# Kernel tuning notes

Measured on AMD Instinct MI355X. Metric: run time of the kernel, lower is better.

## Reference

```python
import math
import jax, jax.numpy as jnp
import numpy as np

B, T, C, H = 4, 2048, 1024, 16
D = C // H  # head dim = 64


def setup_inputs() -> dict:
    key = jax.random.key(0)
    ks = jax.random.split(key, 5)
    s = 0.02  # trunc_normal-like init scale
    return {
        "x":  jax.random.normal(ks[0], (B, T, C), dtype=jnp.float32),
        "wq": jax.random.normal(ks[1], (C, C), dtype=jnp.float32) * s,
        "bq": jnp.zeros((C,), dtype=jnp.float32),
        "wk": jax.random.normal(ks[2], (C, C), dtype=jnp.float32) * s,
        "bk": jnp.zeros((C,), dtype=jnp.float32),
        "wv": jax.random.normal(ks[3], (C, C), dtype=jnp.float32) * s,
        "bv": jnp.zeros((C,), dtype=jnp.float32),
        "wp": jax.random.normal(ks[4], (C, C), dtype=jnp.float32) * s,
        "bp": jnp.zeros((C,), dtype=jnp.float32),
    }


def reference(x, wq, bq, wk, bk, wv, bv, wp, bp):
    b, t, c = x.shape
    # QKV projections -> (B, H, T, D)
    q = (x @ wq + bq).reshape(b, t, H, D).transpose(0, 2, 1, 3)
    k = (x @ wk + bk).reshape(b, t, H, D).transpose(0, 2, 1, 3)
    v = (x @ wv + bv).reshape(b, t, H, D).transpose(0, 2, 1, 3)
    present = jnp.stack((k, v))  # (2, B, H, T, D)
    # scaled dot-product with causal mask (layer_past is None path)
    att = jnp.einsum('bhqd,bhkd->bhqk', q, k) * (1.0 / math.sqrt(D))
    causal = jnp.tril(jnp.ones((t, t), dtype=bool))  # (T, T)
    att = jnp.where(causal[None, None], att, -jnp.inf)
    att = jax.nn.softmax(att, axis=-1)
    # dropout prob = 0.0 (eval) -> identity
    y = jnp.einsum('bhqk,bhkd->bhqd', att, v)
    y = y.transpose(0, 2, 1, 3).reshape(b, t, c)
    y = y @ wp + bp
    return (y, present)
```

## Files before the change

kernel.cpp:

```cpp
#include <hip/hip_runtime.h>
#include <hip/hip_bf16.h>
#include <stdint.h>

typedef unsigned short u16;
typedef __bf16 bf16x8 __attribute__((ext_vector_type(8)));
typedef float f32x4 __attribute__((ext_vector_type(4)));

#define BB 4
#define TT 2048
#define CC 1024
#define HH 16
#define DD 64

__device__ __forceinline__ u16 f2bf(float f) {
  union { float f; unsigned int u; } v; v.f = f;
  unsigned int u = v.u;
  unsigned int r = (u + 0x7fffu + ((u >> 16) & 1u)) >> 16;
  return (u16)r;
}

__device__ __forceinline__ void async_copy16(const void* g, void* l) {
  __builtin_amdgcn_global_load_lds(
      (const __attribute__((address_space(1))) void*)g,
      (__attribute__((address_space(3))) void*)l, 16, 0, 0);
}

__global__ __launch_bounds__(256) void k_cast_x(const float* __restrict__ x,
                                                u16* __restrict__ xb) {
  int i = (blockIdx.x * 256 + threadIdx.x) * 4;
  float4 f = *reinterpret_cast<const float4*>(x + i);
  ushort4 o;
  o.x = f2bf(f.x); o.y = f2bf(f.y); o.z = f2bf(f.z); o.w = f2bf(f.w);
  *reinterpret_cast<ushort4*>(xb + i) = o;
}

__global__ __launch_bounds__(256) void k_transpose_w(
    const float* __restrict__ w0, const float* __restrict__ w1,
    const float* __restrict__ w2, const float* __restrict__ w3,
    u16* __restrict__ t0, u16* __restrict__ t1,
    u16* __restrict__ t2, u16* __restrict__ t3) {
  const float* w = blockIdx.z == 0 ? w0 : blockIdx.z == 1 ? w1 : blockIdx.z == 2 ? w2 : w3;
  u16* t = blockIdx.z == 0 ? t0 : blockIdx.z == 1 ? t1 : blockIdx.z == 2 ? t2 : t3;
  __shared__ u16 tile[32][33];
  int tx = threadIdx.x, ty = threadIdx.y;
  int k0 = blockIdx.x * 32, n0 = blockIdx.y * 32;
#pragma unroll
  for (int r = 0; r < 4; r++)
    tile[ty + r * 8][tx] = f2bf(w[(size_t)(k0 + ty + r * 8) * CC + n0 + tx]);
  __syncthreads();
#pragma unroll
  for (int r = 0; r < 4; r++)
    t[(size_t)(n0 + ty + r * 8) * CC + k0 + tx] = tile[tx][ty + r * 8];
}

__global__ __launch_bounds__(256) void k_transpose_v(
    const float* __restrict__ out_v, u16* __restrict__ vbt) {
  int tb = blockIdx.x * 64;
  int bh = blockIdx.y;
  const float* src = out_v + (size_t)bh * TT * DD;
  u16* dst = vbt + (size_t)bh * TT * DD;
  __shared__ u16 tile[64][65];
  int tid = threadIdx.x;
#pragma unroll
  for (int p = 0; p < 4; p++) {
    int c = p * 256 + tid;
    int t = c >> 4, d0 = (c & 15) * 4;
    float4 f = *reinterpret_cast<const float4*>(src + (size_t)(tb + t) * DD + d0);
    tile[t][d0 + 0] = f2bf(f.x);
    tile[t][d0 + 1] = f2bf(f.y);
    tile[t][d0 + 2] = f2bf(f.z);
    tile[t][d0 + 3] = f2bf(f.w);
  }
  __syncthreads();
#pragma unroll
  for (int p = 0; p < 2; p++) {
    int c = p * 256 + tid;
    int d = c >> 3, t0 = (c & 7) * 8;
    ushort4 lo, hi;
    lo.x = tile[t0 + 0][d]; lo.y = tile[t0 + 1][d];
    lo.z = tile[t0 + 2][d]; lo.w = tile[t0 + 3][d];
    hi.x = tile[t0 + 4][d]; hi.y = tile[t0 + 5][d];
    hi.z = tile[t0 + 6][d]; hi.w = tile[t0 + 7][d];
    u16* o = dst + (size_t)d * TT + tb + t0;
    *reinterpret_cast<ushort4*>(o) = lo;
    *reinterpret_cast<ushort4*>(o + 4) = hi;
  }
}

#define GEMM_PROLOGUE()                                                        \
  int tid = threadIdx.x;                                                       \
  int lane = tid & 63;                                                         \
  int wave = tid >> 6;                                                         \
  int l15 = lane & 15, quad = lane >> 4;                                       \
  int wave_m = wave & 1, wave_n = wave >> 1;                                   \
  __shared__ u16 lA[128 * 32];                                                 \
  __shared__ u16 lB[128 * 32];                                                 \
  f32x4 acc[4][4] = {};                                                        \
  for (int k0 = 0; k0 < CC; k0 += 32) {                                        \
    __syncthreads();                                                           \
    _Pragma("unroll")                                                          \
    for (int r = 0; r < 2; r++) {                                              \
      int c = r * 256 + tid;                                                   \
      int row = c >> 2, col8 = (c & 3) * 8;                                    \
      async_copy16(A + (size_t)(tile_m + row) * CC + k0 + col8, &lA[c * 8]);   \
    }                                                                          \
    _Pragma("unroll")                                                          \
    for (int r = 0; r < 2; r++) {                                              \
      int c = r * 256 + tid;                                                   \
      int row = c >> 2, col8 = (c & 3) * 8;                                    \
      async_copy16(Bt + (size_t)(tile_n + row) * CC + k0 + col8, &lB[c * 8]);  \
    }                                                                          \
    __syncthreads();                                                           \
    bf16x8 af[4], bfr[4];                                                      \
    _Pragma("unroll")                                                          \
    for (int i = 0; i < 4; i++)                                                \
      af[i] = *reinterpret_cast<const bf16x8*>(                                \
          &lA[(wave_m * 64 + i * 16 + l15) * 32 + quad * 8]);                  \
    _Pragma("unroll")                                                          \
    for (int j = 0; j < 4; j++)                                                \
      bfr[j] = *reinterpret_cast<const bf16x8*>(                               \
          &lB[(wave_n * 64 + j * 16 + l15) * 32 + quad * 8]);                  \
    _Pragma("unroll")                                                          \
    for (int i = 0; i < 4; i++)                                                \
      _Pragma("unroll")                                                        \
      for (int j = 0; j < 4; j++)                                              \
        acc[i][j] =                                                            \
            __builtin_amdgcn_mfma_f32_16x16x32_bf16(af[i], bfr[j], acc[i][j],  \
                                                    0, 0, 0);                  \
  }

__global__ __launch_bounds__(256) void k_gemm_qkv(
    const u16* __restrict__ xb,
    const u16* __restrict__ wtq, const u16* __restrict__ wtk, const u16* __restrict__ wtv,
    const float* __restrict__ bq, const float* __restrict__ bk, const float* __restrict__ bv,
    u16* __restrict__ qb, u16* __restrict__ kb,
    float* __restrict__ out_k, float* __restrict__ out_v) {
  int mat = blockIdx.z;
  const u16* A = xb;
  const u16* Bt = mat == 0 ? wtq : mat == 1 ? wtk : wtv;
  const float* bias = mat == 0 ? bq : mat == 1 ? bk : bv;
  int tile_m = blockIdx.x * 128;
  int tile_n = blockIdx.y * 128;

  GEMM_PROLOGUE()

#pragma unroll
  for (int j = 0; j < 4; j++) {
    int n = tile_n + wave_n * 64 + j * 16 + l15;
    int h = n >> 6, d = n & 63;
    float bias_n = bias[n];
#pragma unroll
    for (int i = 0; i < 4; i++) {
#pragma unroll
      for (int r = 0; r < 4; r++) {
        int m = tile_m + wave_m * 64 + i * 16 + quad * 4 + r;
        int b = m >> 11, t = m & 2047;
        float val = acc[i][j][r] + bias_n;
        size_t idx = (((size_t)(b * HH + h)) * TT + t) * DD + d;
        if (mat == 0) {
          qb[idx] = f2bf(val);
        } else if (mat == 1) {
          out_k[idx] = val;
          kb[idx] = f2bf(val);
        } else {
          out_v[idx] = val;
        }
      }
    }
  }
}

__global__ __launch_bounds__(256) void k_gemm_proj(
    const u16* __restrict__ yb, const u16* __restrict__ wtp,
    const float* __restrict__ bp, float* __restrict__ out) {
  const u16* A = yb;
  const u16* Bt = wtp;
  int tile_m = blockIdx.x * 128;
  int tile_n = blockIdx.y * 128;

  GEMM_PROLOGUE()

#pragma unroll
  for (int j = 0; j < 4; j++) {
    int n = tile_n + wave_n * 64 + j * 16 + l15;
    float bias_n = bp[n];
#pragma unroll
    for (int i = 0; i < 4; i++) {
#pragma unroll
      for (int r = 0; r < 4; r++) {
        int m = tile_m + wave_m * 64 + i * 16 + quad * 4 + r;
        out[(size_t)m * CC + n] = acc[i][j][r] + bias_n;
      }
    }
  }
}

__global__ __launch_bounds__(256) void k_attn(
    const u16* __restrict__ qb, const u16* __restrict__ kbuf,
    const u16* __restrict__ vtb, u16* __restrict__ yatt) {
  int qpair = blockIdx.x;
  int bh = blockIdx.y;
  int tid = threadIdx.x;
  int lane = tid & 63;
  int wave = tid >> 6;
  int l15 = lane & 15, quad = lane >> 4;

  const u16* Q = qb + (size_t)bh * TT * DD;
  const u16* K = kbuf + (size_t)bh * TT * DD;
  const u16* Vt = vtb + (size_t)bh * TT * DD;

  __shared__ u16 kl[2][64 * 64];
  __shared__ u16 vl[2][64 * 64];
  __shared__ u16 pl[4][16 * 64];
  u16* plw = pl[wave];

  int h = bh & 15, b = bh >> 4;

  int c0 = tid, c1 = tid + 256;
  int r0 = c0 >> 3, e0 = (((c0 & 7) * 16) ^ ((r0 & 7) << 4)) >> 1;
  int r1 = c1 >> 3, e1 = (((c1 & 7) * 16) ^ ((r1 & 7) << 4)) >> 1;

  auto stage = [&](int buf, int kb0) {
    async_copy16(K + (size_t)(kb0 + r0) * DD + e0, &kl[buf][c0 * 8]);
    async_copy16(K + (size_t)(kb0 + r1) * DD + e1, &kl[buf][c1 * 8]);
    async_copy16(Vt + (size_t)r0 * TT + kb0 + e0, &vl[buf][c0 * 8]);
    async_copy16(Vt + (size_t)r1 * TT + kb0 + e1, &vl[buf][c1 * 8]);
  };

#pragma unroll
  for (int side = 0; side < 2; side++) {
    int qt = side == 0 ? qpair : 31 - qpair;

    int qr = qt * 64 + wave * 16 + l15;
    bf16x8 qf0 = *reinterpret_cast<const bf16x8*>(Q + (size_t)qr * DD + quad * 8);
    bf16x8 qf1 = *reinterpret_cast<const bf16x8*>(Q + (size_t)qr * DD + 32 + quad * 8);

    f32x4 o_acc[4] = {};
    float m_run[4], l_run[4];
#pragma unroll
    for (int r = 0; r < 4; r++) { m_run[r] = -1e30f; l_run[r] = 0.f; }

    stage(0, 0);

    for (int kblk = 0; kblk <= qt; kblk++) {
      int cur = kblk & 1;
      if (kblk < qt) {
        stage(cur ^ 1, (kblk + 1) * 64);
        asm volatile("s_waitcnt vmcnt(4)" ::: "memory");
      } else {
        asm volatile("s_waitcnt vmcnt(0)" ::: "memory");
      }
      __builtin_amdgcn_sched_barrier(0);
      __builtin_amdgcn_s_barrier();
      __builtin_amdgcn_sched_barrier(0);

      f32x4 s_acc[4];
#pragma unroll
      for (int nb = 0; nb < 4; nb++) {
        int krow = nb * 16 + l15;
        int xr = (krow & 7) << 4;
        const u16* kp = &kl[cur][krow * 64];
        bf16x8 kf0 = *reinterpret_cast<const bf16x8*>(kp + (((quad * 16) ^ xr) >> 1));
        bf16x8 kf1 = *reinterpret_cast<const bf16x8*>(kp + (((64 + quad * 16) ^ xr) >> 1));
        f32x4 z = {};
        z = __builtin_amdgcn_mfma_f32_16x16x32_bf16(qf0, kf0, z, 0, 0, 0);
        z = __builtin_amdgcn_mfma_f32_16x16x32_bf16(qf1, kf1, z, 0, 0, 0);
        s_acc[nb] = z;
      }

      float p[4][4];
      float newm[4];
      if (kblk == qt) {
#pragma unroll
        for (int r = 0; r < 4; r++) {
          int qg = qt * 64 + wave * 16 + quad * 4 + r;
          float mx = -1e30f;
#pragma unroll
          for (int nb = 0; nb < 4; nb++) {
            int kg = kblk * 64 + nb * 16 + l15;
            float s = s_acc[nb][r] * 0.125f;
            s = (kg <= qg) ? s : -1e30f;
            p[nb][r] = s;
            mx = fmaxf(mx, s);
          }
          newm[r] = mx;
        }
      } else {
#pragma unroll
        for (int r = 0; r < 4; r++) {
          float mx = -1e30f;
#pragma unroll
          for (int nb = 0; nb < 4; nb++) {
            float s = s_acc[nb][r] * 0.125f;
            p[nb][r] = s;
            mx = fmaxf(mx, s);
          }
          newm[r] = mx;
        }
      }
#pragma unroll
      for (int off = 1; off < 16; off <<= 1) {
#pragma unroll
        for (int r = 0; r < 4; r++)
          newm[r] = fmaxf(newm[r], __shfl_xor(newm[r], off, 64));
      }

      float alpha[4], rs[4];
#pragma unroll
      for (int r = 0; r < 4; r++) {
        float mnew = fmaxf(m_run[r], newm[r]);
        alpha[r] = __expf(m_run[r] - mnew);
        m_run[r] = mnew;
        float local = 0.f;
#pragma unroll
        for (int nb = 0; nb < 4; nb++) {
          float e = __expf(p[nb][r] - mnew);
          p[nb][r] = e;
          local += e;
        }
        rs[r] = local;
      }
#pragma unroll
      for (int off = 1; off < 16; off <<= 1) {
#pragma unroll
        for (int r = 0; r < 4; r++)
          rs[r] += __shfl_xor(rs[r], off, 64);
      }
#pragma unroll
      for (int r = 0; r < 4; r++) {
        l_run[r] = l_run[r] * alpha[r] + rs[r];
#pragma unroll
        for (int db = 0; db < 4; db++) o_acc[db][r] *= alpha[r];
      }

#pragma unroll
      for (int nb = 0; nb < 4; nb++)
#pragma unroll
        for (int r = 0; r < 4; r++) {
          int prow = quad * 4 + r;
          int pcol = ((nb * 16 + l15) * 2) ^ ((prow & 7) << 4);
          plw[prow * 64 + (pcol >> 1)] = f2bf(p[nb][r]);
        }

#pragma unroll
      for (int half = 0; half < 2; half++) {
        int pxr = (l15 & 7) << 4;
        bf16x8 pf = *reinterpret_cast<const bf16x8*>(
            plw + l15 * 64 + (((half * 64 + quad * 16) ^ pxr) >> 1));
#pragma unroll
        for (int db = 0; db < 4; db++) {
          int vrow = db * 16 + l15;
          bf16x8 vf = *reinterpret_cast<const bf16x8*>(
              &vl[cur][vrow * 64] + (((half * 64 + quad * 16) ^ ((vrow & 7) << 4)) >> 1));
          o_acc[db] = __builtin_amdgcn_mfma_f32_16x16x32_bf16(pf, vf, o_acc[db], 0, 0, 0);
        }
      }

      __builtin_amdgcn_sched_barrier(0);
      __builtin_amdgcn_s_barrier();
    }

#pragma unroll
    for (int r = 0; r < 4; r++) {
      float inv = 1.0f / l_run[r];
      int tq = qt * 64 + wave * 16 + quad * 4 + r;
#pragma unroll
      for (int db = 0; db < 4; db++) {
        int d = db * 16 + l15;
        yatt[((size_t)(b * TT + tq)) * CC + h * DD + d] = f2bf(o_acc[db][r] * inv);
      }
    }
  }
}

extern "C" void kernel_launch(void* const* d_in, const int* in_sizes, int n_in,
                              void* d_out, int out_size, void* d_ws, size_t ws_size,
                              hipStream_t stream) {
  const float* x  = (const float*)d_in[0];
  const float* wq = (const float*)d_in[1];
  const float* bq = (const float*)d_in[2];
  const float* wk = (const float*)d_in[3];
  const float* bk = (const float*)d_in[4];
  const float* wv = (const float*)d_in[5];
  const float* bv = (const float*)d_in[6];
  const float* wp = (const float*)d_in[7];
  const float* bp = (const float*)d_in[8];

  float* out_y = (float*)d_out;
  float* out_k = out_y + (size_t)BB * TT * CC;
  float* out_v = out_k + (size_t)BB * HH * TT * DD;

  u16* xb  = (u16*)d_ws;
  u16* wtq = xb + (size_t)BB * TT * CC;
  u16* wtk = wtq + (size_t)CC * CC;
  u16* wtv = wtk + (size_t)CC * CC;
  u16* wtp = wtv + (size_t)CC * CC;
  u16* qb  = wtp + (size_t)CC * CC;
  u16* kb  = qb + (size_t)BB * TT * CC;
  u16* vbt = kb + (size_t)BB * TT * CC;
  u16* yb  = vbt + (size_t)BB * TT * CC;

  k_cast_x<<<(BB * TT * CC) / 1024, 256, 0, stream>>>(x, xb);
  k_transpose_w<<<dim3(CC / 32, CC / 32, 4), dim3(32, 8), 0, stream>>>(
      wq, wk, wv, wp, wtq, wtk, wtv, wtp);
  k_gemm_qkv<<<dim3(BB * TT / 128, CC / 128, 3), 256, 0, stream>>>(
      xb, wtq, wtk, wtv, bq, bk, bv, qb, kb, out_k, out_v);
  k_transpose_v<<<dim3(TT / 64, BB * HH), 256, 0, stream>>>(out_v, vbt);
  k_attn<<<dim3(16, BB * HH), 256, 0, stream>>>(qb, kb, vbt, yb);
  k_gemm_proj<<<dim3(BB * TT / 128, CC / 128), 256, 0, stream>>>(yb, wtp, bp, out_y);
}
```

Baseline: 388.6 us.

## Widen attention KV tile to 128, fold scale into Q, skip lazy rescale

Attention now walks keys in 128-wide tiles instead of 64, halving loop iterations, barriers and softmax reductions per query tile. The 1/sqrt(D) scale is folded into Q when the projection writes it. The online-softmax rescale of the accumulator is skipped unless the running max grows by more than 8 anywhere in the wave. s_setprio is raised around MFMA bursts. The trade-off is double the LDS footprint, which can lower occupancy. On the diagonal tile, causal masking now wastes up to half of a 128-wide tile's work.

```diff
diff --git a/kernel.cpp b/kernel.cpp
--- a/kernel.cpp
+++ b/kernel.cpp
@@ -158,7 +158,7 @@
         float val = acc[i][j][r] + bias_n;
         size_t idx = (((size_t)(b * HH + h)) * TT + t) * DD + d;
         if (mat == 0) {
-          qb[idx] = f2bf(val);
+          qb[idx] = f2bf(val * 0.125f);
         } else if (mat == 1) {
           out_k[idx] = val;
           kb[idx] = f2bf(val);
@@ -209,27 +209,38 @@
   const u16* K = kbuf + (size_t)bh * TT * DD;
   const u16* Vt = vtb + (size_t)bh * TT * DD;
 
-  __shared__ u16 kl[2][64 * 64];
-  __shared__ u16 vl[2][64 * 64];
-  __shared__ u16 pl[4][16 * 64];
+  __shared__ u16 kl[2][128 * 64];
+  __shared__ u16 vl[2][64 * 128];
+  __shared__ u16 pl[4][16 * 128];
   u16* plw = pl[wave];
 
   int h = bh & 15, b = bh >> 4;
 
-  int c0 = tid, c1 = tid + 256;
-  int r0 = c0 >> 3, e0 = (((c0 & 7) * 16) ^ ((r0 & 7) << 4)) >> 1;
-  int r1 = c1 >> 3, e1 = (((c1 & 7) * 16) ^ ((r1 & 7) << 4)) >> 1;
+  int kr[4], ke[4], vr[4], ve[4];
+#pragma unroll
+  for (int i = 0; i < 4; i++) {
+    int c = tid + i * 256;
+    kr[i] = c >> 3;
+    ke[i] = ((((c & 7) * 16) ^ ((kr[i] & 7) << 4)) >> 1);
+    vr[i] = c >> 4;
+    ve[i] = ((((c & 15) * 16) ^ ((vr[i] & 7) << 4)) >> 1);
+  }
 
   auto stage = [&](int buf, int kb0) {
-    async_copy16(K + (size_t)(kb0 + r0) * DD + e0, &kl[buf][c0 * 8]);
-    async_copy16(K + (size_t)(kb0 + r1) * DD + e1, &kl[buf][c1 * 8]);
-    async_copy16(Vt + (size_t)r0 * TT + kb0 + e0, &vl[buf][c0 * 8]);
-    async_copy16(Vt + (size_t)r1 * TT + kb0 + e1, &vl[buf][c1 * 8]);
+#pragma unroll
+    for (int i = 0; i < 4; i++)
+      async_copy16(K + (size_t)(kb0 + kr[i]) * DD + ke[i],
+                   &kl[buf][(tid + i * 256) * 8]);
+#pragma unroll
+    for (int i = 0; i < 4; i++)
+      async_copy16(Vt + (size_t)vr[i] * TT + kb0 + ve[i],
+                   &vl[buf][(tid + i * 256) * 8]);
   };
 
 #pragma unroll
   for (int side = 0; side < 2; side++) {
     int qt = side == 0 ? qpair : 31 - qpair;
+    int nkit = (qt >> 1) + 1;
 
     int qr = qt * 64 + wave * 16 + l15;
     bf16x8 qf0 = *reinterpret_cast<const bf16x8*>(Q + (size_t)qr * DD + quad * 8);
@@ -242,11 +253,11 @@
 
     stage(0, 0);
 
-    for (int kblk = 0; kblk <= qt; kblk++) {
-      int cur = kblk & 1;
-      if (kblk < qt) {
-        stage(cur ^ 1, (kblk + 1) * 64);
-        asm volatile("s_waitcnt vmcnt(4)" ::: "memory");
+    for (int kit = 0; kit < nkit; kit++) {
+      int cur = kit & 1;
+      if (kit < nkit - 1) {
+        stage(cur ^ 1, (kit + 1) * 128);
+        asm volatile("s_waitcnt vmcnt(8)" ::: "memory");
       } else {
         asm volatile("s_waitcnt vmcnt(0)" ::: "memory");
       }
@@ -254,9 +265,10 @@
       __builtin_amdgcn_s_barrier();
       __builtin_amdgcn_sched_barrier(0);
 
-      f32x4 s_acc[4];
-#pragma unroll
-      for (int nb = 0; nb < 4; nb++) {
+      f32x4 s_acc[8];
+      __builtin_amdgcn_s_setprio(1);
+#pragma unroll
+      for (int nb = 0; nb < 8; nb++) {
         int krow = nb * 16 + l15;
         int xr = (krow & 7) << 4;
         const u16* kp = &kl[cur][krow * 64];
@@ -267,18 +279,19 @@
         z = __builtin_amdgcn_mfma_f32_16x16x32_bf16(qf1, kf1, z, 0, 0, 0);
         s_acc[nb] = z;
       }
-
-      float p[4][4];
+      __builtin_amdgcn_s_setprio(0);
+
+      float p[8][4];
       float newm[4];
-      if (kblk == qt) {
+      if (kit == nkit - 1) {
 #pragma unroll
         for (int r = 0; r < 4; r++) {
           int qg = qt * 64 + wave * 16 + quad * 4 + r;
           float mx = -1e30f;
 #pragma unroll
-          for (int nb = 0; nb < 4; nb++) {
-            int kg = kblk * 64 + nb * 16 + l15;
-            float s = s_acc[nb][r] * 0.125f;
+          for (int nb = 0; nb < 8; nb++) {
+            int kg = kit * 128 + nb * 16 + l15;
+            float s = s_acc[nb][r];
             s = (kg <= qg) ? s : -1e30f;
             p[nb][r] = s;
             mx = fmaxf(mx, s);
@@ -290,8 +303,8 @@
         for (int r = 0; r < 4; r++) {
           float mx = -1e30f;
 #pragma unroll
-          for (int nb = 0; nb < 4; nb++) {
-            float s = s_acc[nb][r] * 0.125f;
+          for (int nb = 0; nb < 8; nb++) {
+            float s = s_acc[nb][r];
             p[nb][r] = s;
             mx = fmaxf(mx, s);
           }
@@ -305,16 +318,27 @@
           newm[r] = fmaxf(newm[r], __shfl_xor(newm[r], off, 64));
       }
 
-      float alpha[4], rs[4];
+      float growth = fmaxf(fmaxf(newm[0] - m_run[0], newm[1] - m_run[1]),
+                           fmaxf(newm[2] - m_run[2], newm[3] - m_run[3]));
+      if (!__all(growth <= 8.0f)) {
+#pragma unroll
+        for (int r = 0; r < 4; r++) {
+          float mnew = fmaxf(m_run[r], newm[r]);
+          float alpha = __expf(m_run[r] - mnew);
+          m_run[r] = mnew;
+          l_run[r] *= alpha;
+#pragma unroll
+          for (int db = 0; db < 4; db++) o_acc[db][r] *= alpha;
+        }
+      }
+
+      float rs[4];
 #pragma unroll
       for (int r = 0; r < 4; r++) {
-        float mnew = fmaxf(m_run[r], newm[r]);
-        alpha[r] = __expf(m_run[r] - mnew);
-        m_run[r] = mnew;
         float local = 0.f;
 #pragma unroll
-        for (int nb = 0; nb < 4; nb++) {
-          float e = __expf(p[nb][r] - mnew);
+        for (int nb = 0; nb < 8; nb++) {
+          float e = __expf(p[nb][r] - m_run[r]);
           p[nb][r] = e;
           local += e;
         }
@@ -327,37 +351,36 @@
           rs[r] += __shfl_xor(rs[r], off, 64);
       }
 #pragma unroll
-      for (int r = 0; r < 4; r++) {
-        l_run[r] = l_run[r] * alpha[r] + rs[r];
-#pragma unroll
-        for (int db = 0; db < 4; db++) o_acc[db][r] *= alpha[r];
-      }
-
-#pragma unroll
-      for (int nb = 0; nb < 4; nb++)
+      for (int r = 0; r < 4; r++) l_run[r] += rs[r];
+
+#pragma unroll
+      for (int nb = 0; nb < 8; nb++)
 #pragma unroll
         for (int r = 0; r < 4; r++) {
           int prow = quad * 4 + r;
           int pcol = ((nb * 16 + l15) * 2) ^ ((prow & 7) << 4);
-          plw[prow * 64 + (pcol >> 1)] = f2bf(p[nb][r]);
-        }
-
-#pragma unroll
-      for (int half = 0; half < 2; half++) {
+          plw[prow * 128 + (pcol >> 1)] = f2bf(p[nb][r]);
+        }
+
+      __builtin_amdgcn_s_setprio(1);
+#pragma unroll
+      for (int hh = 0; hh < 4; hh++) {
         int pxr = (l15 & 7) << 4;
         bf16x8 pf = *reinterpret_cast<const bf16x8*>(
-            plw + l15 * 64 + (((half * 64 + quad * 16) ^ pxr) >> 1));
+            plw + l15 * 128 + (((hh * 64 + quad * 16) ^ pxr) >> 1));
 #pragma unroll
         for (int db = 0; db < 4; db++) {
           int vrow = db * 16 + l15;
           bf16x8 vf = *reinterpret_cast<const bf16x8*>(
-              &vl[cur][vrow * 64] + (((half * 64 + quad * 16) ^ ((vrow & 7) << 4)) >> 1));
+              &vl[cur][vrow * 128] + (((hh * 64 + quad * 16) ^ ((vrow & 7) << 4)) >> 1));
           o_acc[db] = __builtin_amdgcn_mfma_f32_16x16x32_bf16(pf, vf, o_acc[db], 0, 0, 0);
         }
       }
+      __builtin_amdgcn_s_setprio(0);
 
       __builtin_amdgcn_sched_barrier(0);
       __builtin_amdgcn_s_barrier();
+      __builtin_amdgcn_sched_barrier(0);
     }
 
 #pragma unroll
```

Result: faster. 372.4 us (-4.2%).

## Fold softmax scale into Q, use exp2, lazy rescale, setprio around MFMAs

Applied to the files above, without the earlier changes.

Folds 1/sqrt(D)*log2(e) into Q when it is written in the QKV GEMM epilogue, so the attention loop drops its per-score multiply and can call the native exp2 instruction. Adds a lazy-rescale path that skips the running-max update and the O/l rescale unless some row's max grows by more than 8 in log2 units. Also switches the P store to a hardware bf16 conversion and raises wave priority around the MFMA blocks. The trade-off is a wave-uniform branch, plus unnormalised exponentials that can reach 2^8 and may lose some bf16 precision.

```diff
diff --git a/kernel.cpp b/kernel.cpp
--- a/kernel.cpp
+++ b/kernel.cpp
@@ -11,6 +11,8 @@
 #define CC 1024
 #define HH 16
 #define DD 64
+
+#define QSCALE 0.18033688011112042f
 
 __device__ __forceinline__ u16 f2bf(float f) {
   union { float f; unsigned int u; } v; v.f = f;
@@ -158,7 +160,7 @@
         float val = acc[i][j][r] + bias_n;
         size_t idx = (((size_t)(b * HH + h)) * TT + t) * DD + d;
         if (mat == 0) {
-          qb[idx] = f2bf(val);
+          qb[idx] = f2bf(val * QSCALE);
         } else if (mat == 1) {
           out_k[idx] = val;
           kb[idx] = f2bf(val);
@@ -213,6 +215,7 @@
   __shared__ u16 vl[2][64 * 64];
   __shared__ u16 pl[4][16 * 64];
   u16* plw = pl[wave];
+  __bf16* plb = reinterpret_cast<__bf16*>(plw);
 
   int h = bh & 15, b = bh >> 4;
 
@@ -255,6 +258,7 @@
       __builtin_amdgcn_sched_barrier(0);
 
       f32x4 s_acc[4];
+      __builtin_amdgcn_s_setprio(1);
 #pragma unroll
       for (int nb = 0; nb < 4; nb++) {
         int krow = nb * 16 + l15;
@@ -267,6 +271,7 @@
         z = __builtin_amdgcn_mfma_f32_16x16x32_bf16(qf1, kf1, z, 0, 0, 0);
         s_acc[nb] = z;
       }
+      __builtin_amdgcn_s_setprio(0);
 
       float p[4][4];
       float newm[4];
@@ -278,7 +283,7 @@
 #pragma unroll
           for (int nb = 0; nb < 4; nb++) {
             int kg = kblk * 64 + nb * 16 + l15;
-            float s = s_acc[nb][r] * 0.125f;
+            float s = s_acc[nb][r];
             s = (kg <= qg) ? s : -1e30f;
             p[nb][r] = s;
             mx = fmaxf(mx, s);
@@ -291,7 +296,7 @@
           float mx = -1e30f;
 #pragma unroll
           for (int nb = 0; nb < 4; nb++) {
-            float s = s_acc[nb][r] * 0.125f;
+            float s = s_acc[nb][r];
             p[nb][r] = s;
             mx = fmaxf(mx, s);
           }
@@ -305,16 +310,27 @@
           newm[r] = fmaxf(newm[r], __shfl_xor(newm[r], off, 64));
       }
 
-      float alpha[4], rs[4];
+      float growth = fmaxf(fmaxf(newm[0] - m_run[0], newm[1] - m_run[1]),
+                           fmaxf(newm[2] - m_run[2], newm[3] - m_run[3]));
+      if (!__all(growth <= 8.0f)) {
+#pragma unroll
+        for (int r = 0; r < 4; r++) {
+          float mnew = fmaxf(m_run[r], newm[r]);
+          float alpha = __builtin_amdgcn_exp2f(m_run[r] - mnew);
+          m_run[r] = mnew;
+          l_run[r] *= alpha;
+#pragma unroll
+          for (int db = 0; db < 4; db++) o_acc[db][r] *= alpha;
+        }
+      }
+
+      float rs[4];
 #pragma unroll
       for (int r = 0; r < 4; r++) {
-        float mnew = fmaxf(m_run[r], newm[r]);
-        alpha[r] = __expf(m_run[r] - mnew);
-        m_run[r] = mnew;
         float local = 0.f;
 #pragma unroll
         for (int nb = 0; nb < 4; nb++) {
-          float e = __expf(p[nb][r] - mnew);
+          float e = __builtin_amdgcn_exp2f(p[nb][r] - m_run[r]);
           p[nb][r] = e;
           local += e;
         }
@@ -327,11 +343,7 @@
           rs[r] += __shfl_xor(rs[r], off, 64);
       }
 #pragma unroll
-      for (int r = 0; r < 4; r++) {
-        l_run[r] = l_run[r] * alpha[r] + rs[r];
-#pragma unroll
-        for (int db = 0; db < 4; db++) o_acc[db][r] *= alpha[r];
-      }
+      for (int r = 0; r < 4; r++) l_run[r] += rs[r];
 
 #pragma unroll
       for (int nb = 0; nb < 4; nb++)
@@ -339,9 +351,10 @@
         for (int r = 0; r < 4; r++) {
           int prow = quad * 4 + r;
           int pcol = ((nb * 16 + l15) * 2) ^ ((prow & 7) << 4);
-          plw[prow * 64 + (pcol >> 1)] = f2bf(p[nb][r]);
-        }
-
+          plb[prow * 64 + (pcol >> 1)] = (__bf16)p[nb][r];
+        }
+
+      __builtin_amdgcn_s_setprio(1);
 #pragma unroll
       for (int half = 0; half < 2; half++) {
         int pxr = (l15 & 7) << 4;
@@ -355,6 +368,7 @@
           o_acc[db] = __builtin_amdgcn_mfma_f32_16x16x32_bf16(pf, vf, o_acc[db], 0, 0, 0);
         }
       }
+      __builtin_amdgcn_s_setprio(0);
 
       __builtin_amdgcn_sched_barrier(0);
       __builtin_amdgcn_s_barrier();
```

After: 386.3 us. No clear change (-0.6%).
